# Kernel tuning notes

Hardware: AMD Instinct MI355X
Metric: run time of the kernel (lower is better)

The kernel has to match this reference:

```python
import jax, jax.numpy as jnp
import numpy as np
import math

HEAD = 4
D_MODEL = 128
N_NODES = 2048
SEQ_LEN = 1
D_K = D_MODEL // HEAD
BATCH = 64


def conv1x1_relu(x, w, b):
    # x: [B, C, N, L], w: [O, C], b: [O]  (1x1 Conv2d + ReLU; dropout is identity in eval)
    return jax.nn.relu(jnp.einsum('oc,bcnl->bonl', w, x) + b[None, :, None, None])


def setup_inputs() -> dict:
    key = jax.random.key(0)
    ks = jax.random.split(key, 12)
    s = 0.05
    return {
        'x': jax.random.normal(ks[0], (BATCH, D_MODEL, N_NODES, SEQ_LEN), jnp.float32),
        'q_w': jax.random.normal(ks[1], (D_MODEL, D_MODEL), jnp.float32) * s,
        'q_b': jnp.zeros((D_MODEL,), jnp.float32),
        'v_w': jax.random.normal(ks[2], (D_MODEL, D_MODEL), jnp.float32) * s,
        'v_b': jnp.zeros((D_MODEL,), jnp.float32),
        'c_w': jax.random.normal(ks[3], (D_MODEL, D_MODEL), jnp.float32) * s,
        'c_b': jnp.zeros((D_MODEL,), jnp.float32),
        'memory': jax.random.normal(ks[4], (HEAD, SEQ_LEN, N_NODES, D_K), jnp.float32) * s,
        'nodevec1': jax.random.normal(ks[5], (N_NODES, 10), jnp.float32),
        'nodevec2': jax.random.normal(ks[6], (10, N_NODES), jnp.float32),
        'weights_pool': jax.random.normal(ks[7], (SEQ_LEN, 3, 3), jnp.float32) * s,
        'bias_pool': jax.random.normal(ks[8], (N_NODES, D_K), jnp.float32) * s,
        'aff_w': jnp.ones((D_MODEL, N_NODES, SEQ_LEN), jnp.float32),
        'aff_b': jnp.zeros((D_MODEL, N_NODES, SEQ_LEN), jnp.float32),
    }


def reference(x, q_w, q_b, v_w, v_b, c_w, c_b, memory, nodevec1, nodevec2,
              weights_pool, bias_pool, aff_w, aff_b):
    B = x.shape[0]
    scale = math.sqrt(D_K)

    query = conv1x1_relu(x, q_w, q_b)
    value = conv1x1_relu(x, v_w, v_b)

    # [B, d_model, N, L] -> [B, h, d_k, N, L] -> [B, h, L, N, d_k]
    def split_heads(t):
        return t.reshape(B, HEAD, D_K, N_NODES, SEQ_LEN).transpose(0, 1, 4, 3, 2)

    query = split_heads(query)
    value = split_heads(value)

    key_ = jax.nn.softmax(memory / scale, axis=-1)      # [h, L, N, d_k]
    query = jax.nn.softmax(query / scale, axis=-1)      # [B, h, L, N, d_k]

    Aapt = jax.nn.softmax(jax.nn.relu(nodevec1 @ nodevec2), axis=-1)  # [N, N]

    kv = jnp.einsum('hlnx,bhlny->bhlxy', key_, value)          # [B,h,L,d_k,d_k]
    attn_qkv = jnp.einsum('bhlnx,bhlxy->bhlny', query, kv)     # [B,h,L,N,d_k]

    weights = jnp.einsum('nm,dio->nio', Aapt, weights_pool)    # [N,3,3]
    bias_dyn = Aapt @ bias_pool                                # [N,d_k]
    attn_dyn = jnp.einsum('bhlnc,nio->bhlnc', value, weights) + bias_dyn[None, None, None, :, :]

    out = attn_qkv + attn_dyn                                  # [B,h,L,N,d_k]
    out = out.transpose(0, 1, 4, 3, 2).reshape(B, D_MODEL, N_NODES, SEQ_LEN)
    out = conv1x1_relu(out, c_w, c_b)

    # num_nodes (2048) not in [170, 358, 5] -> affine-residual branch runs
    out = out * aff_w[None] + aff_b[None] + out
    return out
```

## Files before the change

kernel.cpp:

```cpp
#include <hip/hip_runtime.h>

#define NB 64
#define CH 128
#define NNODE 2048
#define NH 4
#define DKK 32
#define INVS 0.17677669529663687f

typedef __bf16 bf16x8 __attribute__((ext_vector_type(8)));
typedef float f32x4 __attribute__((ext_vector_type(4)));
typedef unsigned short ushort_t;

union U16x8 { uint4 u; bf16x8 b; unsigned short s[8]; };
union U16x4 { uint2 u; unsigned short s[4]; };

__device__ inline bf16x8 as_bf16x8(uint4 u){ U16x8 x; x.u = u; return x.b; }
__device__ inline unsigned short f2b(float f){ __bf16 h = (__bf16)f; return __builtin_bit_cast(unsigned short, h); }
__device__ inline float b2f(unsigned short u){ __bf16 h = __builtin_bit_cast(__bf16, u); return (float)h; }

__global__ __launch_bounds__(256) void k0_prep(const float* __restrict__ qw,
    const float* __restrict__ vw, const float* __restrict__ cw,
    const float* __restrict__ memory, const float* __restrict__ bias_pool,
    ushort_t* __restrict__ wqb, ushort_t* __restrict__ wvb, ushort_t* __restrict__ wcb,
    ushort_t* __restrict__ keysT, float* __restrict__ bias_dyn,
    ushort_t* __restrict__ bpT)
{
  int gid = blockIdx.x * 256 + threadIdx.x;
  if (gid < 16384) { wqb[gid] = f2b(qw[gid]); wvb[gid] = f2b(vw[gid]); wcb[gid] = f2b(cw[gid]); }
  bias_dyn[gid] = 0.f;
  { int k = gid >> 11, m = gid & 2047;
    bpT[gid] = f2b(bias_pool[m * 32 + k]); }
  if (gid < 8192) {
    int h = gid >> 11, n = gid & 2047;
    const float* src = memory + (size_t)gid * 32;
    float v[32]; float m = -1e30f;
    #pragma unroll
    for (int i = 0; i < 32; ++i) { v[i] = src[i] * INVS; m = fmaxf(m, v[i]); }
    float s = 0.f;
    #pragma unroll
    for (int i = 0; i < 32; ++i) { v[i] = __expf(v[i] - m); s += v[i]; }
    float inv = 1.f / s;
    #pragma unroll
    for (int i = 0; i < 32; ++i)
      keysT[(size_t)(h * 32 + i) * 2048 + n] = f2b(v[i] * inv);
  }
}

__global__ __launch_bounds__(256) void kb1(const float* __restrict__ nv1,
    const float* __restrict__ nv2, ushort_t* __restrict__ Ebuf)
{
  int n = blockIdx.x; int tid = threadIdx.x;
  float a1[10];
  #pragma unroll
  for (int d = 0; d < 10; ++d) a1[d] = nv1[n * 10 + d];
  int m0 = tid * 8;
  float s[8];
  #pragma unroll
  for (int j = 0; j < 8; ++j) s[j] = 0.f;
  #pragma unroll
  for (int d = 0; d < 10; ++d) {
    const float* p = nv2 + d * 2048 + m0;
    float4 u = *(const float4*)p; float4 v = *(const float4*)(p + 4);
    s[0] += a1[d] * u.x; s[1] += a1[d] * u.y; s[2] += a1[d] * u.z; s[3] += a1[d] * u.w;
    s[4] += a1[d] * v.x; s[5] += a1[d] * v.y; s[6] += a1[d] * v.z; s[7] += a1[d] * v.w;
  }
  float e[8]; float sum = 0.f;
  #pragma unroll
  for (int j = 0; j < 8; ++j) { e[j] = __expf(fmaxf(s[j], 0.f)); sum += e[j]; }
  #pragma unroll
  for (int d = 1; d < 64; d <<= 1) sum += __shfl_xor(sum, d);
  __shared__ float red[4];
  if ((tid & 63) == 0) red[tid >> 6] = sum;
  __syncthreads();
  float inv = 1.f / (red[0] + red[1] + red[2] + red[3]);
  U16x8 o;
  #pragma unroll
  for (int j = 0; j < 8; ++j) o.s[j] = f2b(e[j] * inv);
  *(uint4*)(Ebuf + (size_t)n * 2048 + m0) = o.u;
}

__global__ __launch_bounds__(256) void kb2(const ushort_t* __restrict__ Ebuf,
    const ushort_t* __restrict__ bpT, float* __restrict__ bias_dyn)
{
  int bid = blockIdx.x;
  int n0 = (bid >> 3) * 128;
  int m0 = (bid & 7) * 256;
  int tid = threadIdx.x; int wv = tid >> 6; int lane = tid & 63;
  int quad = lane >> 4; int l16 = lane & 15;
  int r0 = n0 + 32 * wv;
  f32x4 zero4 = {0.f,0.f,0.f,0.f};
  f32x4 acc[2][2];
  acc[0][0] = zero4; acc[0][1] = zero4; acc[1][0] = zero4; acc[1][1] = zero4;
  for (int ks = 0; ks < 256; ks += 32) {
    int mb = m0 + ks + 8 * quad;
    bf16x8 a0 = *(const bf16x8*)(Ebuf + (size_t)(r0 + l16) * 2048 + mb);
    bf16x8 a1 = *(const bf16x8*)(Ebuf + (size_t)(r0 + 16 + l16) * 2048 + mb);
    bf16x8 b0 = *(const bf16x8*)(bpT + (size_t)l16 * 2048 + mb);
    bf16x8 b1 = *(const bf16x8*)(bpT + (size_t)(16 + l16) * 2048 + mb);
    acc[0][0] = __builtin_amdgcn_mfma_f32_16x16x32_bf16(a0, b0, acc[0][0], 0, 0, 0);
    acc[0][1] = __builtin_amdgcn_mfma_f32_16x16x32_bf16(a0, b1, acc[0][1], 0, 0, 0);
    acc[1][0] = __builtin_amdgcn_mfma_f32_16x16x32_bf16(a1, b0, acc[1][0], 0, 0, 0);
    acc[1][1] = __builtin_amdgcn_mfma_f32_16x16x32_bf16(a1, b1, acc[1][1], 0, 0, 0);
  }
  #pragma unroll
  for (int rt = 0; rt < 2; ++rt)
    #pragma unroll
    for (int ct = 0; ct < 2; ++ct)
      #pragma unroll
      for (int r = 0; r < 4; ++r)
        atomicAdd(bias_dyn + (size_t)(r0 + 16*rt + 4*quad + r) * 32 + 16*ct + l16,
                  acc[rt][ct][r]);
}

__global__ __launch_bounds__(256) void k1_qv(const float* __restrict__ x,
    const ushort_t* __restrict__ wqb, const ushort_t* __restrict__ wvb,
    const float* __restrict__ qbias, const float* __restrict__ vbias,
    ushort_t* __restrict__ QsT, ushort_t* __restrict__ VT)
{
  int bid = blockIdx.x; int b = bid >> 5; int n0 = (bid & 31) * 64;
  int tid = threadIdx.x; int wv = tid >> 6; int lane = tid & 63;
  int quad = lane >> 4; int l16 = lane & 15;
  __shared__ __align__(16) ushort_t XT[64][136];
  __shared__ __align__(16) ushort_t QO[64][136];

  uint4 wq[2][4], wvv[2][4];
  #pragma unroll
  for (int ct = 0; ct < 2; ++ct)
    #pragma unroll
    for (int k0 = 0; k0 < 4; ++k0) {
      int off = (32 * wv + 16 * ct + l16) * 128 + 32 * k0 + 8 * quad;
      wq[ct][k0]  = *(const uint4*)(wqb + off);
      wvv[ct][k0] = *(const uint4*)(wvb + off);
    }
  float4 qb4[2], vb4[2];
  #pragma unroll
  for (int ct = 0; ct < 2; ++ct) {
    qb4[ct] = *(const float4*)(qbias + 32 * wv + 16 * ct + 4 * quad);
    vb4[ct] = *(const float4*)(vbias + 32 * wv + 16 * ct + 4 * quad);
  }

  #pragma unroll
  for (int p = 0; p < 2; ++p) {
    int c4 = 4 * ((tid >> 4) + 16 * p);
    int n4 = 4 * (tid & 15);
    float4 r[4];
    #pragma unroll
    for (int j = 0; j < 4; ++j)
      r[j] = *(const float4*)(x + (size_t)(b * 128 + c4 + j) * 2048 + n0 + n4);
    #pragma unroll
    for (int i = 0; i < 4; ++i) {
      U16x4 w;
      w.s[0] = f2b(((const float*)&r[0])[i]);
      w.s[1] = f2b(((const float*)&r[1])[i]);
      w.s[2] = f2b(((const float*)&r[2])[i]);
      w.s[3] = f2b(((const float*)&r[3])[i]);
      *(uint2*)&XT[n4 + i][c4] = w.u;
    }
  }
  __syncthreads();

  f32x4 zero4 = {0.f,0.f,0.f,0.f};
  f32x4 av[4][2];

  #pragma unroll
  for (int nt = 0; nt < 4; ++nt) {
    f32x4 aq[2]; aq[0] = zero4; aq[1] = zero4;
    f32x4 avv[2]; avv[0] = zero4; avv[1] = zero4;
    #pragma unroll
    for (int k0 = 0; k0 < 4; ++k0) {
      bf16x8 bfrag = *(const bf16x8*)&XT[16 * nt + l16][32 * k0 + 8 * quad];
      #pragma unroll
      for (int ct = 0; ct < 2; ++ct) {
        aq[ct]  = __builtin_amdgcn_mfma_f32_16x16x32_bf16(as_bf16x8(wq[ct][k0]),  bfrag, aq[ct],  0, 0, 0);
        avv[ct] = __builtin_amdgcn_mfma_f32_16x16x32_bf16(as_bf16x8(wvv[ct][k0]), bfrag, avv[ct], 0, 0, 0);
      }
    }
    float sq[2][4]; float mx = -1e30f;
    #pragma unroll
    for (int ct = 0; ct < 2; ++ct)
      #pragma unroll
      for (int r = 0; r < 4; ++r) {
        sq[ct][r] = fmaxf(aq[ct][r] + ((const float*)&qb4[ct])[r], 0.f) * INVS;
        mx = fmaxf(mx, sq[ct][r]);
      }
    mx = fmaxf(mx, __shfl_xor(mx, 16));
    mx = fmaxf(mx, __shfl_xor(mx, 32));
    float sum = 0.f;
    #pragma unroll
    for (int ct = 0; ct < 2; ++ct)
      #pragma unroll
      for (int r = 0; r < 4; ++r) { sq[ct][r] = __expf(sq[ct][r] - mx); sum += sq[ct][r]; }
    sum += __shfl_xor(sum, 16);
    sum += __shfl_xor(sum, 32);
    float inv = 1.f / sum;
    #pragma unroll
    for (int ct = 0; ct < 2; ++ct) {
      U16x4 w;
      #pragma unroll
      for (int r = 0; r < 4; ++r) w.s[r] = f2b(sq[ct][r] * inv);
      *(uint2*)&QO[16 * nt + l16][32 * wv + 16 * ct + 4 * quad] = w.u;
    }
    av[nt][0] = avv[0]; av[nt][1] = avv[1];
  }
  __syncthreads();

  #pragma unroll
  for (int nt = 0; nt < 4; ++nt)
    #pragma unroll
    for (int ct = 0; ct < 2; ++ct) {
      U16x4 w;
      #pragma unroll
      for (int r = 0; r < 4; ++r)
        w.s[r] = f2b(fmaxf(av[nt][ct][r] + ((const float*)&vb4[ct])[r], 0.f));
      *(uint2*)&XT[16 * nt + l16][32 * wv + 16 * ct + 4 * quad] = w.u;
    }
  __syncthreads();

  #pragma unroll
  for (int j = 0; j < 4; ++j) {
    int id = tid + 256 * j; int n = id >> 4; int u = id & 15;
    size_t go = (size_t)(b * 2048 + n0 + n) * 128 + 8 * u;
    *(uint4*)(QsT + go) = *(uint4*)&QO[n][8 * u];
    *(uint4*)(VT  + go) = *(uint4*)&XT[n][8 * u];
  }
}

__global__ __launch_bounds__(256) void k2_kv(const ushort_t* __restrict__ keysT,
    const ushort_t* __restrict__ VT, float* __restrict__ kvp)
{
  int bid = blockIdx.x; int b = bid >> 3; int nb = (bid & 7) * 256;
  int tid = threadIdx.x; int wv = tid >> 6; int lane = tid & 63;
  int quad = lane >> 4; int l16 = lane & 15;
  __shared__ __align__(16) ushort_t Vraw[128][136];

  f32x4 zero4 = {0.f,0.f,0.f,0.f};
  f32x4 acc[2][2];
  acc[0][0] = zero4; acc[0][1] = zero4; acc[1][0] = zero4; acc[1][1] = zero4;

  for (int chunk = 0; chunk < 2; ++chunk) {
    int nc = nb + 128 * chunk;
    if (chunk) __syncthreads();
    #pragma unroll
    for (int p = 0; p < 8; ++p) {
      int id = tid + 256 * p; int n = id >> 4; int g = id & 15;
      *(uint4*)&Vraw[n][8 * g] = *(const uint4*)(VT + (size_t)(b * 2048 + nc + n) * 128 + 8 * g);
    }
    __syncthreads();
    const ushort_t* kT = keysT + (size_t)(wv * 32) * 2048 + nc;
    #pragma unroll
    for (int ks = 0; ks < 4; ++ks) {
      int k0 = 32 * ks + 8 * quad;
      bf16x8 a0 = *(const bf16x8*)(kT + (size_t)l16 * 2048 + k0);
      bf16x8 a1 = *(const bf16x8*)(kT + (size_t)(16 + l16) * 2048 + k0);
      U16x8 b0, b1;
      #pragma unroll
      for (int j = 0; j < 8; ++j) {
        b0.s[j] = Vraw[k0 + j][32 * wv + l16];
        b1.s[j] = Vraw[k0 + j][32 * wv + 16 + l16];
      }
      acc[0][0] = __builtin_amdgcn_mfma_f32_16x16x32_bf16(a0, b0.b, acc[0][0], 0, 0, 0);
      acc[0][1] = __builtin_amdgcn_mfma_f32_16x16x32_bf16(a0, b1.b, acc[0][1], 0, 0, 0);
      acc[1][0] = __builtin_amdgcn_mfma_f32_16x16x32_bf16(a1, b0.b, acc[1][0], 0, 0, 0);
      acc[1][1] = __builtin_amdgcn_mfma_f32_16x16x32_bf16(a1, b1.b, acc[1][1], 0, 0, 0);
    }
  }

  float* dst = kvp + (size_t)bid * 4096 + wv * 1024;
  #pragma unroll
  for (int yt = 0; yt < 2; ++yt)
    #pragma unroll
    for (int xt = 0; xt < 2; ++xt)
      #pragma unroll
      for (int r = 0; r < 4; ++r)
        dst[(16 * yt + l16) * 32 + 16 * xt + 4 * quad + r] = acc[xt][yt][r];
}

__global__ __launch_bounds__(256) void kred(const float* __restrict__ kvp,
    float* __restrict__ kvws)
{
  int gid = blockIdx.x * 256 + threadIdx.x;
  int b = gid >> 12; int i = gid & 4095;
  const float* p = kvp + (size_t)(b * 8) * 4096 + i;
  float s = 0.f;
  #pragma unroll
  for (int t = 0; t < 8; ++t) s += p[t * 4096];
  kvws[gid] = s;
}

__global__ __launch_bounds__(256) void k3_out(const ushort_t* __restrict__ QsT,
    const ushort_t* __restrict__ VT, const float* __restrict__ kvws,
    const float* __restrict__ bias_dyn, const ushort_t* __restrict__ wcb,
    const float* __restrict__ cbias, const float* __restrict__ wpool,
    const float* __restrict__ aff_w, const float* __restrict__ aff_b,
    float* __restrict__ out)
{
  int bid = blockIdx.x; int b = bid >> 5; int n0 = (bid & 31) * 64;
  int tid = threadIdx.x; int wv = tid >> 6; int lane = tid & 63;
  int quad = lane >> 4; int l16 = lane & 15;
  __shared__ __align__(16) ushort_t kvT[4][32][40];
  __shared__ __align__(16) ushort_t MID[64][136];
  __shared__ __align__(16) ushort_t VL[64][132];
  __shared__ __align__(16) float    BD[64][36];

  float Ws = 0.f;
  #pragma unroll
  for (int i = 0; i < 9; ++i) Ws += wpool[i];

  uint4 wc[2][4];
  #pragma unroll
  for (int mt = 0; mt < 2; ++mt)
    #pragma unroll
    for (int k0 = 0; k0 < 4; ++k0)
      wc[mt][k0] = *(const uint4*)(wcb + (32 * wv + 16 * mt + l16) * 128 + 32 * k0 + 8 * quad);

  #pragma unroll
  for (int p = 0; p < 16; ++p) {
    int id = tid + 256 * p;
    kvT[id >> 10][(id >> 5) & 31][id & 31] = f2b(kvws[(size_t)b * 4096 + id]);
  }
  #pragma unroll
  for (int p = 0; p < 4; ++p) {
    int id = tid + 256 * p; int n = id >> 4; int u = id & 15;
    *(uint4*)&VL[n][8 * u] = *(const uint4*)(VT + (size_t)(b * 2048 + n0 + n) * 128 + 8 * u);
  }
  #pragma unroll
  for (int p = 0; p < 2; ++p) {
    int id = tid + 256 * p; int n = id >> 3; int g = id & 7;
    *(float4*)&BD[n][4 * g] = *(const float4*)(bias_dyn + (size_t)(n0 + n) * 32 + 4 * g);
  }
  __syncthreads();

  f32x4 zero4 = {0.f,0.f,0.f,0.f};
  f32x4 acc1[4][2];
  #pragma unroll
  for (int nt = 0; nt < 4; ++nt) { acc1[nt][0] = zero4; acc1[nt][1] = zero4; }
  #pragma unroll
  for (int nt = 0; nt < 4; ++nt) {
    bf16x8 aq = *(const bf16x8*)(QsT + (size_t)(b * 2048 + n0 + 16 * nt + l16) * 128 + 32 * wv + 8 * quad);
    #pragma unroll
    for (int ct = 0; ct < 2; ++ct)
      acc1[nt][ct] = __builtin_amdgcn_mfma_f32_16x16x32_bf16(
          aq, *(const bf16x8*)&kvT[wv][16 * ct + l16][8 * quad], acc1[nt][ct], 0, 0, 0);
  }

  #pragma unroll
  for (int nt = 0; nt < 4; ++nt)
    #pragma unroll
    for (int ct = 0; ct < 2; ++ct)
      #pragma unroll
      for (int r = 0; r < 4; ++r) {
        int nl = 16 * nt + 4 * quad + r;
        int cc = 32 * wv + 16 * ct + l16;
        float v = b2f(VL[nl][cc]);
        float bd = BD[nl][16 * ct + l16];
        MID[nl][cc] = f2b(acc1[nt][ct][r] + Ws * v + bd);
      }
  __syncthreads();

  f32x4 acc2[2][4];
  #pragma unroll
  for (int mt = 0; mt < 2; ++mt)
    #pragma unroll
    for (int nt = 0; nt < 4; ++nt) acc2[mt][nt] = zero4;
  #pragma unroll
  for (int k0 = 0; k0 < 4; ++k0) {
    bf16x8 bb[4];
    #pragma unroll
    for (int nt = 0; nt < 4; ++nt)
      bb[nt] = *(const bf16x8*)&MID[16 * nt + l16][32 * k0 + 8 * quad];
    #pragma unroll
    for (int mt = 0; mt < 2; ++mt)
      #pragma unroll
      for (int nt = 0; nt < 4; ++nt)
        acc2[mt][nt] = __builtin_amdgcn_mfma_f32_16x16x32_bf16(
            as_bf16x8(wc[mt][k0]), bb[nt], acc2[mt][nt], 0, 0, 0);
  }

  #pragma unroll
  for (int mt = 0; mt < 2; ++mt)
    #pragma unroll
    for (int nt = 0; nt < 4; ++nt)
      #pragma unroll
      for (int r = 0; r < 4; ++r) {
        int c_out = 32 * wv + 16 * mt + 4 * quad + r;
        int nn2 = n0 + 16 * nt + l16;
        float yv = fmaxf(acc2[mt][nt][r] + cbias[c_out], 0.f);
        size_t ai = (size_t)c_out * 2048 + nn2;
        float awv = aff_w[ai], abv = aff_b[ai];
        out[(size_t)(b * 128 + c_out) * 2048 + nn2] = yv * awv + abv + yv;
      }
}

extern "C" void kernel_launch(void* const* d_in, const int* in_sizes, int n_in,
                              void* d_out, int out_size, void* d_ws, size_t ws_size,
                              hipStream_t stream)
{
  const float* x      = (const float*)d_in[0];
  const float* qw     = (const float*)d_in[1];
  const float* qb     = (const float*)d_in[2];
  const float* vw     = (const float*)d_in[3];
  const float* vb     = (const float*)d_in[4];
  const float* cw     = (const float*)d_in[5];
  const float* cb     = (const float*)d_in[6];
  const float* memory = (const float*)d_in[7];
  const float* nv1    = (const float*)d_in[8];
  const float* nv2    = (const float*)d_in[9];
  const float* wpool  = (const float*)d_in[10];
  const float* bpool  = (const float*)d_in[11];
  const float* aw     = (const float*)d_in[12];
  const float* ab     = (const float*)d_in[13];
  float* out = (float*)d_out;

  char* ws = (char*)d_ws;
  ushort_t* QsT      = (ushort_t*)(ws);
  ushort_t* VT       = (ushort_t*)(ws + 33554432);
  float*    kvws     = (float*)   (ws + 67108864);
  ushort_t* keysT    = (ushort_t*)(ws + 68157440);
  float*    bias_dyn = (float*)   (ws + 69206016);
  ushort_t* wqb      = (ushort_t*)(ws + 69468160);
  ushort_t* wvb      = (ushort_t*)(ws + 69500928);
  ushort_t* wcb      = (ushort_t*)(ws + 69533696);
  ushort_t* Ebuf     = (ushort_t*)(ws + 69566464);
  ushort_t* bpT      = (ushort_t*)(ws + 77955072);
  float*    kvp      = (float*)Ebuf;

  k0_prep<<<256, 256, 0, stream>>>(qw, vw, cw, memory, bpool, wqb, wvb, wcb,
                                   keysT, bias_dyn, bpT);
  kb1<<<2048, 256, 0, stream>>>(nv1, nv2, Ebuf);
  kb2<<<128, 256, 0, stream>>>(Ebuf, bpT, bias_dyn);
  k1_qv<<<2048, 256, 0, stream>>>(x, wqb, wvb, qb, vb, QsT, VT);
  k2_kv<<<512, 256, 0, stream>>>(keysT, VT, kvp);
  kred<<<1024, 256, 0, stream>>>(kvp, kvws);
  k3_out<<<2048, 256, 0, stream>>>(QsT, VT, kvws, bias_dyn, wcb, cb, wpool, aw, ab, out);
}
```

Measured before the change: 213.3 us.

## Fuse key-value reduction into QV projection kernel and coalesce output epilogue

```diff
diff --git a/kernel.cpp b/kernel.cpp
--- a/kernel.cpp
+++ b/kernel.cpp
@@ -23,11 +23,13 @@
     const float* __restrict__ memory, const float* __restrict__ bias_pool,
     ushort_t* __restrict__ wqb, ushort_t* __restrict__ wvb, ushort_t* __restrict__ wcb,
     ushort_t* __restrict__ keysT, float* __restrict__ bias_dyn,
-    ushort_t* __restrict__ bpT)
+    ushort_t* __restrict__ bpT, float* __restrict__ kvws)
 {
   int gid = blockIdx.x * 256 + threadIdx.x;
   if (gid < 16384) { wqb[gid] = f2b(qw[gid]); wvb[gid] = f2b(vw[gid]); wcb[gid] = f2b(cw[gid]); }
   bias_dyn[gid] = 0.f;
+  { float4 z = {0.f,0.f,0.f,0.f};
+    *(float4*)(kvws + (size_t)gid * 4) = z; }
   { int k = gid >> 11, m = gid & 2047;
     bpT[gid] = f2b(bias_pool[m * 32 + k]); }
   if (gid < 8192) {
@@ -83,15 +85,15 @@
     const ushort_t* __restrict__ bpT, float* __restrict__ bias_dyn)
 {
   int bid = blockIdx.x;
-  int n0 = (bid >> 3) * 128;
-  int m0 = (bid & 7) * 256;
+  int n0 = (bid >> 5) * 128;
+  int m0 = (bid & 31) * 64;
   int tid = threadIdx.x; int wv = tid >> 6; int lane = tid & 63;
   int quad = lane >> 4; int l16 = lane & 15;
   int r0 = n0 + 32 * wv;
   f32x4 zero4 = {0.f,0.f,0.f,0.f};
   f32x4 acc[2][2];
   acc[0][0] = zero4; acc[0][1] = zero4; acc[1][0] = zero4; acc[1][1] = zero4;
-  for (int ks = 0; ks < 256; ks += 32) {
+  for (int ks = 0; ks < 64; ks += 32) {
     int mb = m0 + ks + 8 * quad;
     bf16x8 a0 = *(const bf16x8*)(Ebuf + (size_t)(r0 + l16) * 2048 + mb);
     bf16x8 a1 = *(const bf16x8*)(Ebuf + (size_t)(r0 + 16 + l16) * 2048 + mb);
@@ -112,10 +114,12 @@
                   acc[rt][ct][r]);
 }
 
-__global__ __launch_bounds__(256) void k1_qv(const float* __restrict__ x,
+__global__ __launch_bounds__(256, 4) void k1_qv(const float* __restrict__ x,
     const ushort_t* __restrict__ wqb, const ushort_t* __restrict__ wvb,
     const float* __restrict__ qbias, const float* __restrict__ vbias,
-    ushort_t* __restrict__ QsT, ushort_t* __restrict__ VT)
+    const ushort_t* __restrict__ keysT,
+    ushort_t* __restrict__ QsT, ushort_t* __restrict__ VT,
+    float* __restrict__ kvws)
 {
   int bid = blockIdx.x; int b = bid >> 5; int n0 = (bid & 31) * 64;
   int tid = threadIdx.x; int wv = tid >> 6; int lane = tid & 63;
@@ -123,21 +127,14 @@
   __shared__ __align__(16) ushort_t XT[64][136];
   __shared__ __align__(16) ushort_t QO[64][136];
 
-  uint4 wq[2][4], wvv[2][4];
+  f32x4 zero4 = {0.f,0.f,0.f,0.f};
+
+  uint4 wq[2][4];
   #pragma unroll
   for (int ct = 0; ct < 2; ++ct)
     #pragma unroll
-    for (int k0 = 0; k0 < 4; ++k0) {
-      int off = (32 * wv + 16 * ct + l16) * 128 + 32 * k0 + 8 * quad;
-      wq[ct][k0]  = *(const uint4*)(wqb + off);
-      wvv[ct][k0] = *(const uint4*)(wvb + off);
-    }
-  float4 qb4[2], vb4[2];
-  #pragma unroll
-  for (int ct = 0; ct < 2; ++ct) {
-    qb4[ct] = *(const float4*)(qbias + 32 * wv + 16 * ct + 4 * quad);
-    vb4[ct] = *(const float4*)(vbias + 32 * wv + 16 * ct + 4 * quad);
-  }
+    for (int k0 = 0; k0 < 4; ++k0)
+      wq[ct][k0] = *(const uint4*)(wqb + (32 * wv + 16 * ct + l16) * 128 + 32 * k0 + 8 * quad);
 
   #pragma unroll
   for (int p = 0; p < 2; ++p) {
@@ -159,62 +156,116 @@
   }
   __syncthreads();
 
-  f32x4 zero4 = {0.f,0.f,0.f,0.f};
-  f32x4 av[4][2];
-
-  #pragma unroll
-  for (int nt = 0; nt < 4; ++nt) {
-    f32x4 aq[2]; aq[0] = zero4; aq[1] = zero4;
-    f32x4 avv[2]; avv[0] = zero4; avv[1] = zero4;
-    #pragma unroll
-    for (int k0 = 0; k0 < 4; ++k0) {
-      bf16x8 bfrag = *(const bf16x8*)&XT[16 * nt + l16][32 * k0 + 8 * quad];
+  {
+    float4 qb4[2];
+    #pragma unroll
+    for (int ct = 0; ct < 2; ++ct)
+      qb4[ct] = *(const float4*)(qbias + 32 * wv + 16 * ct + 4 * quad);
+    #pragma unroll
+    for (int nt = 0; nt < 4; ++nt) {
+      f32x4 aq[2]; aq[0] = zero4; aq[1] = zero4;
+      #pragma unroll
+      for (int k0 = 0; k0 < 4; ++k0) {
+        bf16x8 bfrag = *(const bf16x8*)&XT[16 * nt + l16][32 * k0 + 8 * quad];
+        aq[0] = __builtin_amdgcn_mfma_f32_16x16x32_bf16(as_bf16x8(wq[0][k0]), bfrag, aq[0], 0, 0, 0);
+        aq[1] = __builtin_amdgcn_mfma_f32_16x16x32_bf16(as_bf16x8(wq[1][k0]), bfrag, aq[1], 0, 0, 0);
+      }
+      float sq[2][4]; float mx = -1e30f;
+      #pragma unroll
+      for (int ct = 0; ct < 2; ++ct)
+        #pragma unroll
+        for (int r = 0; r < 4; ++r) {
+          sq[ct][r] = fmaxf(aq[ct][r] + ((const float*)&qb4[ct])[r], 0.f) * INVS;
+          mx = fmaxf(mx, sq[ct][r]);
+        }
+      mx = fmaxf(mx, __shfl_xor(mx, 16));
+      mx = fmaxf(mx, __shfl_xor(mx, 32));
+      float sum = 0.f;
+      #pragma unroll
+      for (int ct = 0; ct < 2; ++ct)
+        #pragma unroll
+        for (int r = 0; r < 4; ++r) { sq[ct][r] = __expf(sq[ct][r] - mx); sum += sq[ct][r]; }
+      sum += __shfl_xor(sum, 16);
+      sum += __shfl_xor(sum, 32);
+      float inv = 1.f / sum;
       #pragma unroll
       for (int ct = 0; ct < 2; ++ct) {
-        aq[ct]  = __builtin_amdgcn_mfma_f32_16x16x32_bf16(as_bf16x8(wq[ct][k0]),  bfrag, aq[ct],  0, 0, 0);
-        avv[ct] = __builtin_amdgcn_mfma_f32_16x16x32_bf16(as_bf16x8(wvv[ct][k0]), bfrag, avv[ct], 0, 0, 0);
+        U16x4 w;
+        #pragma unroll
+        for (int r = 0; r < 4; ++r) w.s[r] = f2b(sq[ct][r] * inv);
+        *(uint2*)&QO[16 * nt + l16][32 * wv + 16 * ct + 4 * quad] = w.u;
       }
     }
-    float sq[2][4]; float mx = -1e30f;
-    #pragma unroll
-    for (int ct = 0; ct < 2; ++ct)
-      #pragma unroll
-      for (int r = 0; r < 4; ++r) {
-        sq[ct][r] = fmaxf(aq[ct][r] + ((const float*)&qb4[ct])[r], 0.f) * INVS;
-        mx = fmaxf(mx, sq[ct][r]);
-      }
-    mx = fmaxf(mx, __shfl_xor(mx, 16));
-    mx = fmaxf(mx, __shfl_xor(mx, 32));
-    float sum = 0.f;
-    #pragma unroll
-    for (int ct = 0; ct < 2; ++ct)
-      #pragma unroll
-      for (int r = 0; r < 4; ++r) { sq[ct][r] = __expf(sq[ct][r] - mx); sum += sq[ct][r]; }
-    sum += __shfl_xor(sum, 16);
-    sum += __shfl_xor(sum, 32);
-    float inv = 1.f / sum;
-    #pragma unroll
-    for (int ct = 0; ct < 2; ++ct) {
-      U16x4 w;
-      #pragma unroll
-      for (int r = 0; r < 4; ++r) w.s[r] = f2b(sq[ct][r] * inv);
-      *(uint2*)&QO[16 * nt + l16][32 * wv + 16 * ct + 4 * quad] = w.u;
+  }
+
+  uint2 vout[4][2];
+  {
+    uint4 wvw[2][4];
+    #pragma unroll
+    for (int ct = 0; ct < 2; ++ct)
+      #pragma unroll
+      for (int k0 = 0; k0 < 4; ++k0)
+        wvw[ct][k0] = *(const uint4*)(wvb + (32 * wv + 16 * ct + l16) * 128 + 32 * k0 + 8 * quad);
+    float4 vb4[2];
+    #pragma unroll
+    for (int ct = 0; ct < 2; ++ct)
+      vb4[ct] = *(const float4*)(vbias + 32 * wv + 16 * ct + 4 * quad);
+    #pragma unroll
+    for (int nt = 0; nt < 4; ++nt) {
+      f32x4 av[2]; av[0] = zero4; av[1] = zero4;
+      #pragma unroll
+      for (int k0 = 0; k0 < 4; ++k0) {
+        bf16x8 bfrag = *(const bf16x8*)&XT[16 * nt + l16][32 * k0 + 8 * quad];
+        av[0] = __builtin_amdgcn_mfma_f32_16x16x32_bf16(as_bf16x8(wvw[0][k0]), bfrag, av[0], 0, 0, 0);
+        av[1] = __builtin_amdgcn_mfma_f32_16x16x32_bf16(as_bf16x8(wvw[1][k0]), bfrag, av[1], 0, 0, 0);
+      }
+      #pragma unroll
+      for (int ct = 0; ct < 2; ++ct) {
+        U16x4 w;
+        #pragma unroll
+        for (int r = 0; r < 4; ++r)
+          w.s[r] = f2b(fmaxf(av[ct][r] + ((const float*)&vb4[ct])[r], 0.f));
+        vout[nt][ct] = w.u;
+      }
     }
-    av[nt][0] = avv[0]; av[nt][1] = avv[1];
   }
   __syncthreads();
 
   #pragma unroll
   for (int nt = 0; nt < 4; ++nt)
     #pragma unroll
-    for (int ct = 0; ct < 2; ++ct) {
-      U16x4 w;
-      #pragma unroll
-      for (int r = 0; r < 4; ++r)
-        w.s[r] = f2b(fmaxf(av[nt][ct][r] + ((const float*)&vb4[ct])[r], 0.f));
-      *(uint2*)&XT[16 * nt + l16][32 * wv + 16 * ct + 4 * quad] = w.u;
+    for (int ct = 0; ct < 2; ++ct)
+      *(uint2*)&XT[16 * nt + l16][32 * wv + 16 * ct + 4 * quad] = vout[nt][ct];
+  __syncthreads();
+
+  {
+    f32x4 akv[2][2];
+    akv[0][0] = zero4; akv[0][1] = zero4; akv[1][0] = zero4; akv[1][1] = zero4;
+    #pragma unroll
+    for (int ks = 0; ks < 2; ++ks) {
+      const ushort_t* kp = keysT + (size_t)(32 * wv) * 2048 + n0 + 32 * ks + 8 * quad;
+      bf16x8 ka0 = *(const bf16x8*)(kp + (size_t)l16 * 2048);
+      bf16x8 ka1 = *(const bf16x8*)(kp + (size_t)(16 + l16) * 2048);
+      U16x8 v0, v1;
+      #pragma unroll
+      for (int j = 0; j < 8; ++j) {
+        v0.s[j] = XT[32 * ks + 8 * quad + j][32 * wv + l16];
+        v1.s[j] = XT[32 * ks + 8 * quad + j][32 * wv + 16 + l16];
+      }
+      akv[0][0] = __builtin_amdgcn_mfma_f32_16x16x32_bf16(ka0, v0.b, akv[0][0], 0, 0, 0);
+      akv[0][1] = __builtin_amdgcn_mfma_f32_16x16x32_bf16(ka0, v1.b, akv[0][1], 0, 0, 0);
+      akv[1][0] = __builtin_amdgcn_mfma_f32_16x16x32_bf16(ka1, v0.b, akv[1][0], 0, 0, 0);
+      akv[1][1] = __builtin_amdgcn_mfma_f32_16x16x32_bf16(ka1, v1.b, akv[1][1], 0, 0, 0);
     }
-  __syncthreads();
+    float* kdst = kvws + (size_t)b * 4096 + wv * 1024;
+    #pragma unroll
+    for (int xt = 0; xt < 2; ++xt)
+      #pragma unroll
+      for (int yt = 0; yt < 2; ++yt)
+        #pragma unroll
+        for (int r = 0; r < 4; ++r)
+          atomicAdd(kdst + (16 * yt + l16) * 32 + 16 * xt + 4 * quad + r, akv[xt][yt][r]);
+  }
 
   #pragma unroll
   for (int j = 0; j < 4; ++j) {
@@ -225,69 +276,7 @@
   }
 }
 
-__global__ __launch_bounds__(256) void k2_kv(const ushort_t* __restrict__ keysT,
-    const ushort_t* __restrict__ VT, float* __restrict__ kvp)
-{
-  int bid = blockIdx.x; int b = bid >> 3; int nb = (bid & 7) * 256;
-  int tid = threadIdx.x; int wv = tid >> 6; int lane = tid & 63;
-  int quad = lane >> 4; int l16 = lane & 15;
-  __shared__ __align__(16) ushort_t Vraw[128][136];
-
-  f32x4 zero4 = {0.f,0.f,0.f,0.f};
-  f32x4 acc[2][2];
-  acc[0][0] = zero4; acc[0][1] = zero4; acc[1][0] = zero4; acc[1][1] = zero4;
-
-  for (int chunk = 0; chunk < 2; ++chunk) {
-    int nc = nb + 128 * chunk;
-    if (chunk) __syncthreads();
-    #pragma unroll
-    for (int p = 0; p < 8; ++p) {
-      int id = tid + 256 * p; int n = id >> 4; int g = id & 15;
-      *(uint4*)&Vraw[n][8 * g] = *(const uint4*)(VT + (size_t)(b * 2048 + nc + n) * 128 + 8 * g);
-    }
-    __syncthreads();
-    const ushort_t* kT = keysT + (size_t)(wv * 32) * 2048 + nc;
-    #pragma unroll
-    for (int ks = 0; ks < 4; ++ks) {
-      int k0 = 32 * ks + 8 * quad;
-      bf16x8 a0 = *(const bf16x8*)(kT + (size_t)l16 * 2048 + k0);
-      bf16x8 a1 = *(const bf16x8*)(kT + (size_t)(16 + l16) * 2048 + k0);
-      U16x8 b0, b1;
-      #pragma unroll
-      for (int j = 0; j < 8; ++j) {
-        b0.s[j] = Vraw[k0 + j][32 * wv + l16];
-        b1.s[j] = Vraw[k0 + j][32 * wv + 16 + l16];
-      }
-      acc[0][0] = __builtin_amdgcn_mfma_f32_16x16x32_bf16(a0, b0.b, acc[0][0], 0, 0, 0);
-      acc[0][1] = __builtin_amdgcn_mfma_f32_16x16x32_bf16(a0, b1.b, acc[0][1], 0, 0, 0);
-      acc[1][0] = __builtin_amdgcn_mfma_f32_16x16x32_bf16(a1, b0.b, acc[1][0], 0, 0, 0);
-      acc[1][1] = __builtin_amdgcn_mfma_f32_16x16x32_bf16(a1, b1.b, acc[1][1], 0, 0, 0);
-    }
-  }
-
-  float* dst = kvp + (size_t)bid * 4096 + wv * 1024;
-  #pragma unroll
-  for (int yt = 0; yt < 2; ++yt)
-    #pragma unroll
-    for (int xt = 0; xt < 2; ++xt)
-      #pragma unroll
-      for (int r = 0; r < 4; ++r)
-        dst[(16 * yt + l16) * 32 + 16 * xt + 4 * quad + r] = acc[xt][yt][r];
-}
-
-__global__ __launch_bounds__(256) void kred(const float* __restrict__ kvp,
-    float* __restrict__ kvws)
-{
-  int gid = blockIdx.x * 256 + threadIdx.x;
-  int b = gid >> 12; int i = gid & 4095;
-  const float* p = kvp + (size_t)(b * 8) * 4096 + i;
-  float s = 0.f;
-  #pragma unroll
-  for (int t = 0; t < 8; ++t) s += p[t * 4096];
-  kvws[gid] = s;
-}
-
-__global__ __launch_bounds__(256) void k3_out(const ushort_t* __restrict__ QsT,
+__global__ __launch_bounds__(256, 3) void k3_out(const ushort_t* __restrict__ QsT,
     const ushort_t* __restrict__ VT, const float* __restrict__ kvws,
     const float* __restrict__ bias_dyn, const ushort_t* __restrict__ wcb,
     const float* __restrict__ cbias, const float* __restrict__ wpool,
@@ -297,10 +286,12 @@
   int bid = blockIdx.x; int b = bid >> 5; int n0 = (bid & 31) * 64;
   int tid = threadIdx.x; int wv = tid >> 6; int lane = tid & 63;
   int quad = lane >> 4; int l16 = lane & 15;
-  __shared__ __align__(16) ushort_t kvT[4][32][40];
-  __shared__ __align__(16) ushort_t MID[64][136];
-  __shared__ __align__(16) ushort_t VL[64][132];
-  __shared__ __align__(16) float    BD[64][36];
+  __shared__ __align__(16) char smem[53760];
+  ushort_t (*kvT)[32][40] = (ushort_t(*)[32][40])(smem);
+  ushort_t (*MID)[136]    = (ushort_t(*)[136])(smem + 10240);
+  ushort_t (*VL)[132]     = (ushort_t(*)[132])(smem + 27648);
+  float    (*BD)[36]      = (float(*)[36])(smem + 44544);
+  float    (*OST)[64]     = (float(*)[64])(smem + 10240);
 
   float Ws = 0.f;
   #pragma unroll
@@ -375,7 +366,12 @@
         acc2[mt][nt] = __builtin_amdgcn_mfma_f32_16x16x32_bf16(
             as_bf16x8(wc[mt][k0]), bb[nt], acc2[mt][nt], 0, 0, 0);
   }
-
+  __syncthreads();
+
+  float4 cb4[2];
+  #pragma unroll
+  for (int mt = 0; mt < 2; ++mt)
+    cb4[mt] = *(const float4*)(cbias + 32 * wv + 16 * mt + 4 * quad);
   #pragma unroll
   for (int mt = 0; mt < 2; ++mt)
     #pragma unroll
@@ -383,12 +379,24 @@
       #pragma unroll
       for (int r = 0; r < 4; ++r) {
         int c_out = 32 * wv + 16 * mt + 4 * quad + r;
-        int nn2 = n0 + 16 * nt + l16;
-        float yv = fmaxf(acc2[mt][nt][r] + cbias[c_out], 0.f);
-        size_t ai = (size_t)c_out * 2048 + nn2;
-        float awv = aff_w[ai], abv = aff_b[ai];
-        out[(size_t)(b * 128 + c_out) * 2048 + nn2] = yv * awv + abv + yv;
-      }
+        OST[c_out][16 * nt + l16] = fmaxf(acc2[mt][nt][r] + ((const float*)&cb4[mt])[r], 0.f);
+      }
+  __syncthreads();
+
+  #pragma unroll
+  for (int p = 0; p < 8; ++p) {
+    int id = tid + 256 * p; int c = id >> 4; int g = id & 15;
+    float4 y = *(const float4*)&OST[c][4 * g];
+    size_t ai = (size_t)c * 2048 + n0 + 4 * g;
+    float4 aw4 = *(const float4*)(aff_w + ai);
+    float4 ab4 = *(const float4*)(aff_b + ai);
+    float4 o;
+    o.x = y.x * aw4.x + ab4.x + y.x;
+    o.y = y.y * aw4.y + ab4.y + y.y;
+    o.z = y.z * aw4.z + ab4.z + y.z;
+    o.w = y.w * aw4.w + ab4.w + y.w;
+    *(float4*)(out + (size_t)(b * 128 + c) * 2048 + n0 + 4 * g) = o;
+  }
 }
 
 extern "C" void kernel_launch(void* const* d_in, const int* in_sizes, int n_in,
@@ -422,14 +430,11 @@
   ushort_t* wcb      = (ushort_t*)(ws + 69533696);
   ushort_t* Ebuf     = (ushort_t*)(ws + 69566464);
   ushort_t* bpT      = (ushort_t*)(ws + 77955072);
-  float*    kvp      = (float*)Ebuf;
 
   k0_prep<<<256, 256, 0, stream>>>(qw, vw, cw, memory, bpool, wqb, wvb, wcb,
-                                   keysT, bias_dyn, bpT);
+                                   keysT, bias_dyn, bpT, kvws);
   kb1<<<2048, 256, 0, stream>>>(nv1, nv2, Ebuf);
-  kb2<<<128, 256, 0, stream>>>(Ebuf, bpT, bias_dyn);
-  k1_qv<<<2048, 256, 0, stream>>>(x, wqb, wvb, qb, vb, QsT, VT);
-  k2_kv<<<512, 256, 0, stream>>>(keysT, VT, kvp);
-  kred<<<1024, 256, 0, stream>>>(kvp, kvws);
+  kb2<<<512, 256, 0, stream>>>(Ebuf, bpT, bias_dyn);
+  k1_qv<<<2048, 256, 0, stream>>>(x, wqb, wvb, qb, vb, keysT, QsT, VT, kvws);
   k3_out<<<2048, 256, 0, stream>>>(QsT, VT, kvws, bias_dyn, wcb, cb, wpool, aw, ab, out);
 }
```

Result: slower. 284.6 us (+33.4%).
